# Optimization experiments

Hardware: AMD Instinct MI355X
Metric: run time of the kernel (lower is better)

Reference implementation:

```python
import jax, jax.numpy as jnp
import numpy as np
from jax import lax

NL, HID, DIN, DST, DCONV, DTR = 4, 256, 512, 16, 4, 16  # layers, d_model, expand*d_model, d_state, d_conv, dt_rank
B, H, W = 4, 256, 256


def setup_inputs() -> dict:
    key = jax.random.key(0)
    ks = jax.random.split(key, 8)
    def n(k, s, sc=0.02):
        return jax.random.normal(k, s, dtype=jnp.float32) * sc
    return {
        "x": jax.random.normal(ks[0], (B, 3, H, W), dtype=jnp.float32),
        "conv1_w": n(ks[1], (HID // 2, 3, 3, 3), 0.1), "conv1_b": jnp.zeros((HID // 2,), jnp.float32),
        "gn1_w": jnp.ones((HID // 2,), jnp.float32), "gn1_b": jnp.zeros((HID // 2,), jnp.float32),
        "conv2_w": n(ks[2], (HID, HID // 2, 3, 3), 0.05), "conv2_b": jnp.zeros((HID,), jnp.float32),
        "gn2_w": jnp.ones((HID,), jnp.float32), "gn2_b": jnp.zeros((HID,), jnp.float32),
        "ln_w": jnp.ones((NL, HID), jnp.float32), "ln_b": jnp.zeros((NL, HID), jnp.float32),
        "in_proj_w": n(ks[3], (NL, 2 * DIN, HID)),
        "conv1d_w": n(ks[4], (NL, DIN, 1, DCONV), 0.1), "conv1d_b": jnp.zeros((NL, DIN), jnp.float32),
        "x_proj_w": n(ks[5], (NL, DTR + 2 * DST, DIN)),
        "dt_proj_w": n(ks[6], (NL, DIN, DTR), 0.1),
        "dt_proj_b": jnp.full((NL, DIN), -4.6, dtype=jnp.float32),  # softplus(-4.6) ~ 0.01
        "A_log": jnp.broadcast_to(jnp.log(jnp.arange(1, DST + 1, dtype=jnp.float32)), (NL, DIN, DST)) + jnp.zeros((NL, DIN, DST), jnp.float32),
        "D": jnp.ones((NL, DIN), jnp.float32),
        "out_proj_w": n(ks[7], (NL, HID, DIN)),
    }


def conv2d_s2(x, w, b):
    y = lax.conv_general_dilated(x, w, (2, 2), [(1, 1), (1, 1)],
                                 dimension_numbers=('NCHW', 'OIHW', 'NCHW'))
    return y + b[None, :, None, None]


def group_norm(x, w, b, groups=8, eps=1e-5):
    Bb, C, Hh, Ww = x.shape
    xg = x.reshape(Bb, groups, C // groups, Hh, Ww)
    m = xg.mean((2, 3, 4), keepdims=True)
    v = xg.var((2, 3, 4), keepdims=True)
    xg = (xg - m) * lax.rsqrt(v + eps)
    return xg.reshape(Bb, C, Hh, Ww) * w[None, :, None, None] + b[None, :, None, None]


def layer_norm(x, w, b, eps=1e-5):
    m = x.mean(-1, keepdims=True)
    v = x.var(-1, keepdims=True)
    return (x - m) * lax.rsqrt(v + eps) * w + b


def mamba(x, ipw, cw, cb, xpw, dpw, dpb, A_log, Dp, opw):
    # x: [B, L, HID]
    Bb, L, _ = x.shape
    xz = jnp.einsum('bld,ed->ble', x, ipw)           # [B, L, 2*DIN]
    xc, z = jnp.split(xz, 2, axis=-1)
    # depthwise causal conv1d over L
    u = xc.transpose(0, 2, 1)                        # [B, DIN, L]
    u = lax.conv_general_dilated(u, cw, (1,), [(DCONV - 1, 0)],
                                 dimension_numbers=('NCH', 'OIH', 'NCH'),
                                 feature_group_count=DIN)
    xc = jax.nn.silu(u + cb[None, :, None]).transpose(0, 2, 1)  # [B, L, DIN]
    x_dbl = jnp.einsum('bld,ed->ble', xc, xpw)       # [B, L, DTR+2*DST]
    dt, Bm, Cm = jnp.split(x_dbl, [DTR, DTR + DST], axis=-1)
    delta = jax.nn.softplus(jnp.einsum('blr,dr->bld', dt, dpw) + dpb)  # [B, L, DIN]
    A = -jnp.exp(A_log)                              # [DIN, DST]
    dA = jnp.exp(jnp.einsum('bld,dn->bldn', delta, A))
    dBu = jnp.einsum('bld,bln,bld->bldn', delta, Bm, xc)

    def step(h, inp):
        dA_t, dBu_t, C_t = inp
        h = dA_t * h + dBu_t                         # [B, DIN, DST]
        return h, jnp.einsum('bdn,bn->bd', h, C_t)

    h0 = jnp.zeros((Bb, DIN, DST), x.dtype)
    _, ys = lax.scan(step, h0, (dA.transpose(1, 0, 2, 3), dBu.transpose(1, 0, 2, 3), Cm.transpose(1, 0, 2)))
    y = ys.transpose(1, 0, 2) + xc * Dp              # [B, L, DIN]
    y = y * jax.nn.silu(z)
    return jnp.einsum('bld,ed->ble', y, opw)         # [B, L, HID]


def reference(x, conv1_w, conv1_b, gn1_w, gn1_b, conv2_w, conv2_b, gn2_w, gn2_b,
              ln_w, ln_b, in_proj_w, conv1d_w, conv1d_b, x_proj_w, dt_proj_w,
              dt_proj_b, A_log, D, out_proj_w):
    y = jax.nn.silu(group_norm(conv2d_s2(x, conv1_w, conv1_b), gn1_w, gn1_b))
    y = jax.nn.silu(group_norm(conv2d_s2(y, conv2_w, conv2_b), gn2_w, gn2_b))
    Bb, C, h, w = y.shape
    s = y.reshape(Bb, C, h * w).transpose(0, 2, 1)   # b (h w) c
    for i in range(NL):
        s = s + mamba(layer_norm(s, ln_w[i], ln_b[i]), in_proj_w[i], conv1d_w[i],
                      conv1d_b[i], x_proj_w[i], dt_proj_w[i], dt_proj_b[i],
                      A_log[i], D[i], out_proj_w[i])
    return (s, h, w)
```

## Files before the change

### kernel.cpp

```cpp
#include <hip/hip_runtime.h>
#include <math.h>

#define BB 4
#define C1 128
#define H1 128
#define W1 128
#define C2 256
#define H2 64
#define W2 64
#define LSEQ 4096
#define HID 256
#define DIN 512
#define DST 16
#define DTR 16
#define NL 4
#define NCHUNK 128
#define LCH 32

typedef unsigned short u16;
using short8 = __attribute__((ext_vector_type(8))) short;
using f32x4  = __attribute__((ext_vector_type(4))) float;
using f32x2  = __attribute__((ext_vector_type(2))) float;

static __device__ __forceinline__ float dsilu(float x){
    return x / (1.0f + __expf(-x));
}
static __device__ __forceinline__ u16 f2bf(float f){
    unsigned u = __float_as_uint(f);
    u += 0x7FFF + ((u >> 16) & 1);
    return (u16)(u >> 16);
}
static __device__ __forceinline__ float bf2f(u16 v){
    return __uint_as_float(((unsigned)v) << 16);
}

#define GLL16(g, l) __builtin_amdgcn_global_load_lds( \
    (const __attribute__((address_space(1))) void*)(g), \
    (__attribute__((address_space(3))) void*)(l), 16, 0, 0)

#define VMW4 asm volatile("s_waitcnt vmcnt(4)" ::: "memory")
#define VMW5 asm volatile("s_waitcnt vmcnt(5)" ::: "memory")
#define VMW0 asm volatile("s_waitcnt vmcnt(0)" ::: "memory")

static __device__ __forceinline__ void blockbar(){
    asm volatile("" ::: "memory");
    __builtin_amdgcn_s_barrier();
    asm volatile("" ::: "memory");
}

__global__ void f2bf_kernel(const float* __restrict__ src, u16* __restrict__ dst){
    int idx = blockIdx.x * 256 + threadIdx.x;
    dst[idx] = f2bf(src[idx]);
}
__global__ void wdt_prep_kernel(const float* __restrict__ xpw, const float* __restrict__ dpw,
                                u16* __restrict__ wcomb){
    int idx = blockIdx.x * 256 + threadIdx.x;
    int k = idx & 511;
    int n = (idx >> 9) % 640;
    int layer = idx / (640*512);
    u16 val = 0;
    if(n < 512){
        const float* dp = dpw + ((long)layer*512 + n)*16;
        const float* xp = xpw + (long)layer*48*512 + k;
        float acc = 0.f;
        #pragma unroll
        for(int r = 0; r < 16; ++r) acc = fmaf(dp[r], xp[(long)r*512], acc);
        val = f2bf(acc);
    } else if(n < 544){
        int row = n - 512 + 16;
        val = f2bf(xpw[((long)layer*48 + row)*512 + k]);
    }
    wcomb[((long)layer*640 + n)*512 + k] = val;
}
__global__ void c2w_prep_kernel(const float* __restrict__ src, u16* __restrict__ dst){
    int idx = blockIdx.x * 256 + threadIdx.x;
    int ci = idx & 127, p = (idx >> 7) % 9, co = idx / (9*128);
    int kh = p / 3, kw = p - 3*kh;
    dst[idx] = f2bf(src[((co*128 + ci)*3 + kh)*3 + kw]);
}
__global__ void xt_zero_kernel(unsigned* __restrict__ xt){
    xt[blockIdx.x * 256 + threadIdx.x] = 0;
}

__global__ __launch_bounds__(256) void conv1_kernel(
        const float* __restrict__ x, const float* __restrict__ w,
        const float* __restrict__ bias, float* __restrict__ y){
    __shared__ float xs[9][260];
    int oh = blockIdx.x, b = blockIdx.y;
    int tid = threadIdx.x;
    #pragma unroll
    for(int r = 0; r < 9; ++r){
        int ci = r / 3, kh = r - 3*ci;
        int ih = 2*oh - 1 + kh;
        float v = 0.f;
        if(ih >= 0) v = x[((b*3 + ci)*256 + ih)*256 + tid];
        xs[r][tid + 1] = v;
        if(tid == 0) xs[r][0] = 0.f;
    }
    __syncthreads();
    int co = tid >> 1, h = tid & 1;
    float wr[27];
    #pragma unroll
    for(int j = 0; j < 27; ++j) wr[j] = w[co*27 + j];
    float bz = bias[co];
    long obase = ((long)((b*128 + co)*128 + oh))*128 + h*64;
    #pragma unroll 4
    for(int i = 0; i < 64; ++i){
        int iw0 = 2*(h*64 + i);
        float acc = bz;
        #pragma unroll
        for(int r = 0; r < 9; ++r){
            acc = fmaf(xs[r][iw0+0], wr[r*3+0], acc);
            acc = fmaf(xs[r][iw0+1], wr[r*3+1], acc);
            acc = fmaf(xs[r][iw0+2], wr[r*3+2], acc);
        }
        y[obase + i] = acc;
    }
}

__global__ void zero_stats_kernel(float* __restrict__ stats){
    stats[threadIdx.x] = 0.0f;
}

__global__ void gn_stats_kernel(const float* __restrict__ x, float* __restrict__ stats,
                                int elems_per_group){
    const int EPB = 16384;
    long base = (long)blockIdx.x * EPB;
    int g = (int)(base / elems_per_group);
    float s = 0.f, ss = 0.f;
    for(int j = threadIdx.x; j < EPB; j += 256){
        float v = x[base + j];
        s += v; ss += v*v;
    }
    #pragma unroll
    for(int off = 32; off; off >>= 1){
        s  += __shfl_down(s,  off);
        ss += __shfl_down(ss, off);
    }
    __shared__ float ls[4], lss[4];
    int wid = threadIdx.x >> 6, lane = threadIdx.x & 63;
    if(lane == 0){ ls[wid] = s; lss[wid] = ss; }
    __syncthreads();
    if(threadIdx.x == 0){
        atomicAdd(&stats[g],      ls[0]+ls[1]+ls[2]+ls[3]);
        atomicAdd(&stats[32+g], lss[0]+lss[1]+lss[2]+lss[3]);
    }
}

__global__ void gn1_transform_kernel(const float* __restrict__ y1, const float* __restrict__ stats,
                                     const float* __restrict__ w, const float* __restrict__ bias,
                                     u16* __restrict__ xt){
    __shared__ float tile[32][33];
    int b = blockIdx.z >> 7, ih = blockIdx.z & 127;
    int c0 = blockIdx.y * 32, w0 = blockIdx.x * 32;
    int tx = threadIdx.x, ty = threadIdx.y;
    const float cnt = 16.f * 128.f * 128.f;
    #pragma unroll
    for(int i = 0; i < 4; ++i){
        int ci = c0 + ty + i*8;
        int g = b*8 + (ci >> 4);
        float mean = stats[g] / cnt;
        float var  = stats[32+g] / cnt - mean*mean;
        float rstd = rsqrtf(var + 1e-5f);
        float v = y1[(((long)(b*C1 + ci))*H1 + ih)*W1 + w0 + tx];
        tile[ty + i*8][tx] = dsilu((v - mean) * rstd * w[ci] + bias[ci]);
    }
    __syncthreads();
    #pragma unroll
    for(int i = 0; i < 4; ++i){
        int iwl = ty + i*8;
        xt[((long)(b*130 + ih + 1)*130 + (w0 + iwl + 1))*128 + c0 + tx] = f2bf(tile[tx][iwl]);
    }
}

__global__ __launch_bounds__(256) void conv2gemm_bf16_kernel(
        const u16* __restrict__ xt, const u16* __restrict__ w2,
        const float* __restrict__ bias, float* __restrict__ y2t){
    __shared__ u16 Asm[2][128*32];
    __shared__ u16 Bsm[2][128*32];
    int m0 = blockIdx.x * 128, n0 = blockIdx.y * 128;
    int tid = threadIdx.x;
    long abase[2]; const u16* bbase[2]; int ldst[2];
    #pragma unroll
    for(int it = 0; it < 2; ++it){
        int c = it*256 + tid;
        int r = c >> 2;
        int kq = ((c & 3) ^ ((r >> 1) & 3)) * 8;
        int m = m0 + r;
        int b = m >> 12, oh = (m >> 6) & 63, ow = m & 63;
        abase[it] = ((long)(b*130 + 2*oh)*130 + 2*ow)*128 + kq;
        bbase[it] = w2 + (long)(n0 + r)*1152 + kq;
        ldst[it] = c*8;
    }
    int wave = tid >> 6, lane = tid & 63;
    int wr = wave >> 1, wc = wave & 1;
    int lm = lane & 15, lq = lane >> 4;
    int swq = (lq ^ ((lm >> 1) & 3)) * 8;
    f32x4 acc[4][4] = {};
    #pragma unroll
    for(int it = 0; it < 2; ++it){
        GLL16(xt + abase[it], &Asm[0][ldst[it]]);
        GLL16(bbase[it], &Bsm[0][ldst[it]]);
    }
    for(int kk = 0; kk < 36; ++kk){
        int cur = kk & 1;
        if(kk + 1 < 36){
            int k2 = kk + 1;
            int p = k2 >> 2, cs = k2 & 3;
            int kh = p / 3, kw = p - 3*kh;
            int ao = (kh*130 + kw)*128 + cs*32;
            int bo = k2*32;
            #pragma unroll
            for(int it = 0; it < 2; ++it){
                GLL16(xt + abase[it] + ao, &Asm[cur^1][ldst[it]]);
                GLL16(bbase[it] + bo, &Bsm[cur^1][ldst[it]]);
            }
            VMW4;
        } else {
            VMW0;
        }
        blockbar();
        short8 af[4], bf[4];
        #pragma unroll
        for(int i = 0; i < 4; ++i){
            af[i] = *(const short8*)&Asm[cur][(wr*64 + i*16 + lm)*32 + swq];
            bf[i] = *(const short8*)&Bsm[cur][(wc*64 + i*16 + lm)*32 + swq];
        }
        #pragma unroll
        for(int i = 0; i < 4; ++i)
            #pragma unroll
            for(int j = 0; j < 4; ++j)
                acc[i][j] = __builtin_amdgcn_mfma_f32_16x16x32_bf16(af[i], bf[j], acc[i][j], 0, 0, 0);
        __builtin_amdgcn_sched_barrier(0);
        blockbar();
    }
    #pragma unroll
    for(int i = 0; i < 4; ++i){
        long row = m0 + wr*64 + i*16 + lq*4;
        #pragma unroll
        for(int j = 0; j < 4; ++j){
            int col = n0 + wc*64 + j*16 + lm;
            float bz = bias[col];
            #pragma unroll
            for(int r = 0; r < 4; ++r)
                y2t[(row + r)*256L + col] = acc[i][j][r] + bz;
        }
    }
}

__global__ void gn2t_stats_kernel(const float* __restrict__ y2t, float* __restrict__ stats){
    int b = blockIdx.y;
    long row0 = (long)b*LSEQ + blockIdx.x*64;
    int c = threadIdx.x;
    float s = 0.f, ss = 0.f;
    for(int r = 0; r < 64; ++r){
        float v = y2t[(row0 + r)*C2 + c];
        s += v; ss += v*v;
    }
    #pragma unroll
    for(int off = 16; off; off >>= 1){
        s  += __shfl_down(s,  off);
        ss += __shfl_down(ss, off);
    }
    if((c & 31) == 0){
        int g = b*8 + (c >> 5);
        atomicAdd(&stats[g], s);
        atomicAdd(&stats[32+g], ss);
    }
}

__global__ void gn2t_apply_ln_kernel(const float* __restrict__ y2t, const float* __restrict__ stats,
                                     const float* __restrict__ gw, const float* __restrict__ gb,
                                     const float* __restrict__ lw, const float* __restrict__ lb,
                                     float* __restrict__ s, u16* __restrict__ xln){
    long row = blockIdx.x;
    int c = threadIdx.x;
    int b = (int)(row >> 12);
    int g = b*8 + (c >> 5);
    const float cnt = 32.f * (float)LSEQ;
    float mean = stats[g] / cnt;
    float var  = stats[32+g] / cnt - mean*mean;
    float rstd = rsqrtf(var + 1e-5f);
    float v = dsilu((y2t[row*HID + c] - mean) * rstd * gw[c] + gb[c]);
    s[row*HID + c] = v;
    float sm = v, sq = v*v;
    #pragma unroll
    for(int off = 32; off; off >>= 1){
        sm += __shfl_down(sm, off);
        sq += __shfl_down(sq, off);
    }
    __shared__ float pa[4], pb[4], res[2];
    int wid = c >> 6, lane = c & 63;
    if(lane == 0){ pa[wid] = sm; pb[wid] = sq; }
    __syncthreads();
    if(c == 0){
        float t  = pa[0]+pa[1]+pa[2]+pa[3];
        float tt = pb[0]+pb[1]+pb[2]+pb[3];
        float m2 = t / 256.f;
        float v2 = tt / 256.f - m2*m2;
        res[0] = m2; res[1] = rsqrtf(v2 + 1e-5f);
    }
    __syncthreads();
    xln[row*HID + c] = f2bf((v - res[0]) * res[1] * lw[c] + lb[c]);
}

__global__ __launch_bounds__(256) void gemm_bf16_kernel(
        const u16* __restrict__ A, const u16* __restrict__ B, void* __restrict__ Cv,
        int K, int Nact, int ldc, int mode){
    __shared__ u16 Asm[2][128*32];
    __shared__ u16 Bsm[2][128*32];
    int m0 = blockIdx.x * 128, n0 = blockIdx.y * 128;
    int tid = threadIdx.x;
    int wave = tid >> 6, lane = tid & 63;
    int wr = wave >> 1, wc = wave & 1;
    int lm = lane & 15, lq = lane >> 4;
    int swq = (lq ^ ((lm >> 1) & 3)) * 8;
    const u16* ag[2]; const u16* bg[2]; int ldst[2];
    #pragma unroll
    for(int it = 0; it < 2; ++it){
        int c = it*256 + tid;
        int r = c >> 2;
        int kq = ((c & 3) ^ ((r >> 1) & 3)) * 8;
        ag[it] = A + (long)(m0 + r)*K + kq;
        bg[it] = B + (long)(n0 + r)*K + kq;
        ldst[it] = c*8;
    }
    f32x4 acc[4][4] = {};
    int nk = K >> 5;
    #pragma unroll
    for(int it = 0; it < 2; ++it){
        GLL16(ag[it], &Asm[0][ldst[it]]);
        GLL16(bg[it], &Bsm[0][ldst[it]]);
    }
    for(int kt = 0; kt < nk; ++kt){
        int cur = kt & 1;
        if(kt + 1 < nk){
            int ko = (kt + 1) << 5;
            #pragma unroll
            for(int it = 0; it < 2; ++it){
                GLL16(ag[it] + ko, &Asm[cur^1][ldst[it]]);
                GLL16(bg[it] + ko, &Bsm[cur^1][ldst[it]]);
            }
            VMW4;
        } else {
            VMW0;
        }
        blockbar();
        short8 af[4], bf[4];
        #pragma unroll
        for(int i = 0; i < 4; ++i){
            af[i] = *(const short8*)&Asm[cur][(wr*64 + i*16 + lm)*32 + swq];
            bf[i] = *(const short8*)&Bsm[cur][(wc*64 + i*16 + lm)*32 + swq];
        }
        #pragma unroll
        for(int i = 0; i < 4; ++i)
            #pragma unroll
            for(int j = 0; j < 4; ++j)
                acc[i][j] = __builtin_amdgcn_mfma_f32_16x16x32_bf16(af[i], bf[j], acc[i][j], 0, 0, 0);
        __builtin_amdgcn_sched_barrier(0);
        blockbar();
    }
    #pragma unroll
    for(int i = 0; i < 4; ++i){
        long row = m0 + wr*64 + i*16 + lq*4;
        #pragma unroll
        for(int j = 0; j < 4; ++j){
            int col = n0 + wc*64 + j*16 + lm;
            if(col < Nact){
                #pragma unroll
                for(int r = 0; r < 4; ++r){
                    long idx = (row + r)*(long)ldc + col;
                    if(mode == 2) ((u16*)Cv)[idx] = f2bf(acc[i][j][r]);
                    else          ((float*)Cv)[idx] = acc[i][j][r];
                }
            }
        }
    }
}

__global__ __launch_bounds__(256) void gemm_dtbc_kernel(
        const u16* __restrict__ A, const u16* __restrict__ B,
        const float* __restrict__ dpb, u16* __restrict__ dv,
        float* __restrict__ xdbl32){
    __shared__ u16 Asm[2][128*32];
    __shared__ u16 Bsm[2][128*32];
    int m0 = blockIdx.x * 128, n0 = blockIdx.y * 128;
    int tid = threadIdx.x;
    int wave = tid >> 6, lane = tid & 63;
    int wr = wave >> 1, wc = wave & 1;
    int lm = lane & 15, lq = lane >> 4;
    int swq = (lq ^ ((lm >> 1) & 3)) * 8;
    const u16* ag[2]; const u16* bg[2]; int ldst[2];
    #pragma unroll
    for(int it = 0; it < 2; ++it){
        int c = it*256 + tid;
        int r = c >> 2;
        int kq = ((c & 3) ^ ((r >> 1) & 3)) * 8;
        ag[it] = A + (long)(m0 + r)*512 + kq;
        bg[it] = B + (long)(n0 + r)*512 + kq;
        ldst[it] = c*8;
    }
    f32x4 acc[4][4] = {};
    #pragma unroll
    for(int it = 0; it < 2; ++it){
        GLL16(ag[it], &Asm[0][ldst[it]]);
        GLL16(bg[it], &Bsm[0][ldst[it]]);
    }
    for(int kt = 0; kt < 16; ++kt){
        int cur = kt & 1;
        if(kt + 1 < 16){
            int ko = (kt + 1) << 5;
            #pragma unroll
            for(int it = 0; it < 2; ++it){
                GLL16(ag[it] + ko, &Asm[cur^1][ldst[it]]);
                GLL16(bg[it] + ko, &Bsm[cur^1][ldst[it]]);
            }
            VMW4;
        } else {
            VMW0;
        }
        blockbar();
        short8 af[4], bf[4];
        #pragma unroll
        for(int i = 0; i < 4; ++i){
            af[i] = *(const short8*)&Asm[cur][(wr*64 + i*16 + lm)*32 + swq];
            bf[i] = *(const short8*)&Bsm[cur][(wc*64 + i*16 + lm)*32 + swq];
        }
        #pragma unroll
        for(int i = 0; i < 4; ++i)
            #pragma unroll
            for(int j = 0; j < 4; ++j)
                acc[i][j] = __builtin_amdgcn_mfma_f32_16x16x32_bf16(af[i], bf[j], acc[i][j], 0, 0, 0);
        __builtin_amdgcn_sched_barrier(0);
        blockbar();
    }
    if(n0 < 512){
        #pragma unroll
        for(int i = 0; i < 4; ++i){
            long row = m0 + wr*64 + i*16 + lq*4;
            #pragma unroll
            for(int j = 0; j < 4; ++j){
                int col = n0 + wc*64 + j*16 + lm;
                float bz = dpb[col];
                #pragma unroll
                for(int r = 0; r < 4; ++r){
                    float v = acc[i][j][r] + bz;
                    v = (v > 20.f) ? v : __logf(1.f + __expf(v));
                    dv[(row + r)*512L + col] = f2bf(v);
                }
            }
        }
    } else {
        #pragma unroll
        for(int i = 0; i < 4; ++i){
            long row = m0 + wr*64 + i*16 + lq*4;
            #pragma unroll
            for(int j = 0; j < 4; ++j){
                int lcol = wc*64 + j*16 + lm;
                if(lcol < 32){
                    #pragma unroll
                    for(int r = 0; r < 4; ++r)
                        xdbl32[(row + r)*32L + lcol] = acc[i][j][r];
                }
            }
        }
    }
}

__global__ __launch_bounds__(256) void gemm_out_ln_kernel(
        const u16* __restrict__ A, const u16* __restrict__ B,
        float* __restrict__ s, u16* __restrict__ xln,
        const float* __restrict__ lw, const float* __restrict__ lb){
    __shared__ u16 Asm[2][64*32];
    __shared__ u16 Bsm[2][256*32];
    int m0 = blockIdx.x * 64;
    int tid = threadIdx.x;
    int w = tid >> 6, lane = tid & 63;
    int lm = lane & 15, lq = lane >> 4;
    int swq = (lq ^ ((lm >> 1) & 3)) * 8;
    int ra = tid >> 2;
    int kqa = ((tid & 3) ^ ((ra >> 1) & 3)) * 8;
    const u16* agA = A + (long)(m0 + ra)*512 + kqa;
    int lda = tid*8;
    const u16* bg[4]; int ldb[4];
    #pragma unroll
    for(int it = 0; it < 4; ++it){
        int c = it*256 + tid;
        int r = c >> 2;
        int kq = ((c & 3) ^ ((r >> 1) & 3)) * 8;
        bg[it] = B + (long)r*512 + kq;
        ldb[it] = c*8;
    }
    f32x4 acc[16] = {};
    GLL16(agA, &Asm[0][lda]);
    #pragma unroll
    for(int it = 0; it < 4; ++it)
        GLL16(bg[it], &Bsm[0][ldb[it]]);
    for(int kt = 0; kt < 16; ++kt){
        int cur = kt & 1;
        if(kt + 1 < 16){
            int ko = (kt + 1) << 5;
            GLL16(agA + ko, &Asm[cur^1][lda]);
            #pragma unroll
            for(int it = 0; it < 4; ++it)
                GLL16(bg[it] + ko, &Bsm[cur^1][ldb[it]]);
            VMW5;
        } else {
            VMW0;
        }
        blockbar();
        short8 af = *(const short8*)&Asm[cur][(w*16 + lm)*32 + swq];
        #pragma unroll
        for(int j = 0; j < 16; ++j){
            short8 bf = *(const short8*)&Bsm[cur][(j*16 + lm)*32 + swq];
            acc[j] = __builtin_amdgcn_mfma_f32_16x16x32_bf16(af, bf, acc[j], 0, 0, 0);
        }
        __builtin_amdgcn_sched_barrier(0);
        blockbar();
    }
    int row0 = m0 + w*16 + lq*4;
    float psum[4] = {0.f,0.f,0.f,0.f}, psq[4] = {0.f,0.f,0.f,0.f};
    #pragma unroll
    for(int j = 0; j < 16; ++j){
        int col = j*16 + lm;
        #pragma unroll
        for(int r = 0; r < 4; ++r){
            long idx = (long)(row0 + r)*HID + col;
            float v = s[idx] + acc[j][r];
            acc[j][r] = v;
            s[idx] = v;
            psum[r] += v; psq[r] += v*v;
        }
    }
    #pragma unroll
    for(int mask = 1; mask <= 8; mask <<= 1){
        #pragma unroll
        for(int r = 0; r < 4; ++r){
            psum[r] += __shfl_xor(psum[r], mask);
            psq[r]  += __shfl_xor(psq[r],  mask);
        }
    }
    float mean[4], rstd[4];
    #pragma unroll
    for(int r = 0; r < 4; ++r){
        mean[r] = psum[r] * (1.f/256.f);
        float var = psq[r] * (1.f/256.f) - mean[r]*mean[r];
        rstd[r] = rsqrtf(var + 1e-5f);
    }
    #pragma unroll
    for(int j = 0; j < 16; ++j){
        int col = j*16 + lm;
        float wv = lw[col], bv = lb[col];
        #pragma unroll
        for(int r = 0; r < 4; ++r){
            long idx = (long)(row0 + r)*HID + col;
            xln[idx] = f2bf((acc[j][r] - mean[r]) * rstd[r] * wv + bv);
        }
    }
}

__global__ void conv1d_silu_kernel(const u16* __restrict__ xz, const float* __restrict__ w,
                                   const float* __restrict__ bias, u16* __restrict__ xcv){
    int idx = blockIdx.x * 256 + threadIdx.x;
    int e = idx * 8;
    int d0 = e & 511;
    long m = e >> 9;
    int l = (int)(m & 4095);
    short8 xrow[4];
    const u16* xp = xz + m*(2*DIN) + d0;
    #pragma unroll
    for(int j = 0; j < 4; ++j){
        int t = l - 3 + j;
        if(t >= 0) xrow[j] = *(const short8*)(xp + (long)(j-3)*(2*DIN));
        else       xrow[j] = (short8){0,0,0,0,0,0,0,0};
    }
    float wv[8][4];
    #pragma unroll
    for(int k = 0; k < 8; k += 2){
        float4 a = *(const float4*)(w + (d0+k)*4);
        float4 b = *(const float4*)(w + (d0+k+1)*4);
        wv[k][0]=a.x; wv[k][1]=a.y; wv[k][2]=a.z; wv[k][3]=a.w;
        wv[k+1][0]=b.x; wv[k+1][1]=b.y; wv[k+1][2]=b.z; wv[k+1][3]=b.w;
    }
    float bz[8];
    {
        float4 a = *(const float4*)(bias + d0);
        float4 b = *(const float4*)(bias + d0 + 4);
        bz[0]=a.x; bz[1]=a.y; bz[2]=a.z; bz[3]=a.w;
        bz[4]=b.x; bz[5]=b.y; bz[6]=b.z; bz[7]=b.w;
    }
    short8 out;
    #pragma unroll
    for(int k = 0; k < 8; ++k){
        float acc = bz[k];
        #pragma unroll
        for(int j = 0; j < 4; ++j)
            acc = fmaf(bf2f((u16)xrow[j][k]), wv[k][j], acc);
        out[k] = (short)f2bf(dsilu(acc));
    }
    *(short8*)(xcv + m*DIN + d0) = out;
}

__global__ __launch_bounds__(256) void scan1_kernel(
        const u16* __restrict__ xcvb, const u16* __restrict__ dvin,
        const float* __restrict__ xdbl32, const float* __restrict__ Alog,
        float* __restrict__ aprod, float* __restrict__ hend){
    int d = blockIdx.y * 256 + threadIdx.x;
    int c = blockIdx.x;
    int b = blockIdx.z;
    __shared__ float bm[LCH][16];
    {
        int t = threadIdx.x >> 4, n = threadIdx.x & 15;
        #pragma unroll
        for(int it = 0; it < 2; ++it){
            long p = ((long)(b*LSEQ + c*LCH + t + it*16))*32;
            bm[t + it*16][n] = xdbl32[p + n];
        }
    }
    __syncthreads();
    float An[16];
    #pragma unroll
    for(int n = 0; n < 16; ++n)
        An[n] = -__expf(Alog[d*16 + n]);
    float An0 = An[0];
    bool structural = true;
    #pragma unroll
    for(int n = 0; n < 16; ++n)
        structural = structural && (fabsf(An[n] - (float)(n+1)*An0) <= 1e-3f*(float)(n+1));
    long base = ((long)(b*LSEQ + c*LCH))*DIN + d;
    long ob = (((long)(b*NCHUNK + c))*DIN + d)*16;
    if(structural){
        f32x2 h2[8];
        #pragma unroll
        for(int i = 0; i < 8; ++i) h2[i] = (f32x2){0.f, 0.f};
        float sumdv = 0.f;
        float xv_n = bf2f(xcvb[base]);
        float dv_n = bf2f(dvin[base]);
        for(int t = 0; t < LCH; ++t){
            float xv = xv_n, dv = dv_n;
            if(t + 1 < LCH){
                xv_n = bf2f(xcvb[base + (long)(t+1)*DIN]);
                dv_n = bf2f(dvin[base + (long)(t+1)*DIN]);
            }
            sumdv += dv;
            float db = dv * xv;
            float r1 = __expf(dv * An0);
            float r2 = r1 * r1;
            f32x2 rr = {r2, r2};
            f32x2 e2[8];
            e2[0] = (f32x2){r1, r2};
            #pragma unroll
            for(int i = 1; i < 8; ++i) e2[i] = e2[i-1] * rr;
            f32x2 db2 = {db, db};
            const f32x2* b2 = (const f32x2*)&bm[t][0];
            #pragma unroll
            for(int i = 0; i < 8; ++i) h2[i] = e2[i]*h2[i] + db2*b2[i];
        }
        float R = __expf(An0 * sumdv);
        float Rp = R;
        const float* hp = (const float*)h2;
        #pragma unroll
        for(int n = 0; n < 16; ++n){
            aprod[ob+n] = Rp; Rp *= R;
            hend[ob+n] = hp[n];
        }
    } else {
        float h[16], ap[16];
        #pragma unroll
        for(int n = 0; n < 16; ++n){ h[n] = 0.f; ap[n] = 1.f; }
        for(int t = 0; t < LCH; ++t){
            float dv = bf2f(dvin[base + (long)t*DIN]);
            float db = dv * bf2f(xcvb[base + (long)t*DIN]);
            #pragma unroll
            for(int n = 0; n < 16; ++n){
                float e = __expf(dv * An[n]);
                ap[n] *= e;
                h[n] = fmaf(e, h[n], db * bm[t][n]);
            }
        }
        #pragma unroll
        for(int n = 0; n < 16; ++n){ aprod[ob+n] = ap[n]; hend[ob+n] = h[n]; }
    }
}

__global__ void scan2_kernel(const float* __restrict__ aprod, const float* __restrict__ hend,
                             float* __restrict__ hinit){
    int idx = blockIdx.x * 256 + threadIdx.x;
    int n = idx & 15, d = (idx >> 4) & 511, b = idx >> 13;
    const long stride = (long)DIN * 16;
    long p0 = (((long)(b*NCHUNK))*DIN + d)*16 + n;
    float h = 0.f;
    for(int c = 0; c < NCHUNK; c += 8){
        float a[8], e[8];
        #pragma unroll
        for(int j = 0; j < 8; ++j){
            long p = p0 + (long)(c + j)*stride;
            a[j] = aprod[p]; e[j] = hend[p];
        }
        #pragma unroll
        for(int j = 0; j < 8; ++j){
            hinit[p0 + (long)(c + j)*stride] = h;
            h = fmaf(a[j], h, e[j]);
        }
    }
}

__global__ __launch_bounds__(256) void scan3_kernel(
        const u16* __restrict__ xcvb, const u16* __restrict__ dvin,
        const float* __restrict__ xdbl32, const float* __restrict__ Alog,
        const float* __restrict__ hinit, const float* __restrict__ Dp,
        const u16* __restrict__ xz, u16* __restrict__ yout){
    int d = blockIdx.y * 256 + threadIdx.x;
    int c = blockIdx.x;
    int b = blockIdx.z;
    __shared__ float bm[LCH][16], cm[LCH][16];
    {
        int t = threadIdx.x >> 4, n = threadIdx.x & 15;
        #pragma unroll
        for(int it = 0; it < 2; ++it){
            long p = ((long)(b*LSEQ + c*LCH + t + it*16))*32;
            bm[t + it*16][n] = xdbl32[p + n];
            cm[t + it*16][n] = xdbl32[p + 16 + n];
        }
    }
    __syncthreads();
    float An[16];
    long hb = (((long)(b*NCHUNK + c))*DIN + d)*16;
    #pragma unroll
    for(int n = 0; n < 16; ++n)
        An[n] = -__expf(Alog[d*16 + n]);
    float An0 = An[0];
    bool structural = true;
    #pragma unroll
    for(int n = 0; n < 16; ++n)
        structural = structural && (fabsf(An[n] - (float)(n+1)*An0) <= 1e-3f*(float)(n+1));
    float Dv = Dp[d];
    long base  = ((long)(b*LSEQ + c*LCH))*DIN + d;
    long zbase = ((long)(b*LSEQ + c*LCH))*(2*DIN) + DIN + d;
    if(structural){
        f32x2 h2[8];
        {
            const f32x2* hi = (const f32x2*)&hinit[hb];
            #pragma unroll
            for(int i = 0; i < 8; ++i) h2[i] = hi[i];
        }
        float xv_n = bf2f(xcvb[base]);
        float z_n  = bf2f(xz[zbase]);
        float dv_n = bf2f(dvin[base]);
        for(int t = 0; t < LCH; ++t){
            float xv = xv_n, z = z_n, dv = dv_n;
            if(t + 1 < LCH){
                xv_n = bf2f(xcvb[base + (long)(t+1)*DIN]);
                z_n  = bf2f(xz[zbase + (long)(t+1)*(2*DIN)]);
                dv_n = bf2f(dvin[base + (long)(t+1)*DIN]);
            }
            float db = dv * xv;
            float r1 = __expf(dv * An0);
            float r2 = r1 * r1;
            f32x2 rr = {r2, r2};
            f32x2 e2[8];
            e2[0] = (f32x2){r1, r2};
            #pragma unroll
            for(int i = 1; i < 8; ++i) e2[i] = e2[i-1] * rr;
            f32x2 db2 = {db, db};
            const f32x2* b2 = (const f32x2*)&bm[t][0];
            const f32x2* c2 = (const f32x2*)&cm[t][0];
            f32x2 y2 = {0.f, 0.f};
            #pragma unroll
            for(int i = 0; i < 8; ++i){
                h2[i] = e2[i]*h2[i] + db2*b2[i];
                y2 = y2 + h2[i]*c2[i];
            }
            float y = y2[0] + y2[1];
            y = fmaf(xv, Dv, y);
            yout[base + (long)t*DIN] = f2bf(y * dsilu(z));
        }
    } else {
        float h[16];
        #pragma unroll
        for(int n = 0; n < 16; ++n) h[n] = hinit[hb + n];
        for(int t = 0; t < LCH; ++t){
            float dv = bf2f(dvin[base + (long)t*DIN]);
            float xv = bf2f(xcvb[base + (long)t*DIN]);
            float db = dv * xv;
            float y = 0.f;
            #pragma unroll
            for(int n = 0; n < 16; ++n){
                float e = __expf(dv * An[n]);
                h[n] = fmaf(e, h[n], db * bm[t][n]);
                y = fmaf(h[n], cm[t][n], y);
            }
            y = fmaf(xv, Dv, y);
            float z = bf2f(xz[zbase + (long)t*(2*DIN)]);
            yout[base + (long)t*DIN] = f2bf(y * dsilu(z));
        }
    }
}

__global__ void copyout_kernel(const float* __restrict__ s, float* __restrict__ out, int out_size){
    int idx = blockIdx.x * 256 + threadIdx.x;
    if(idx >= out_size) return;
    out[idx] = (idx < BB*LSEQ*HID) ? s[idx] : 64.0f;
}

extern "C" void kernel_launch(void* const* d_in, const int* in_sizes, int n_in,
                              void* d_out, int out_size, void* d_ws, size_t ws_size,
                              hipStream_t stream){
    const float* x        = (const float*)d_in[0];
    const float* conv1_w  = (const float*)d_in[1];
    const float* conv1_b  = (const float*)d_in[2];
    const float* gn1_w    = (const float*)d_in[3];
    const float* gn1_b    = (const float*)d_in[4];
    const float* conv2_w  = (const float*)d_in[5];
    const float* conv2_b  = (const float*)d_in[6];
    const float* gn2_w    = (const float*)d_in[7];
    const float* gn2_b    = (const float*)d_in[8];
    const float* ln_w     = (const float*)d_in[9];
    const float* ln_b     = (const float*)d_in[10];
    const float* in_proj  = (const float*)d_in[11];
    const float* c1d_w    = (const float*)d_in[12];
    const float* c1d_b    = (const float*)d_in[13];
    const float* x_proj   = (const float*)d_in[14];
    const float* dt_w     = (const float*)d_in[15];
    const float* dt_b     = (const float*)d_in[16];
    const float* A_log    = (const float*)d_in[17];
    const float* Dvec     = (const float*)d_in[18];
    const float* out_proj = (const float*)d_in[19];

    float* ws = (float*)d_ws;
    float* s      = ws;
    u16*   xz_bf  = (u16*)(ws + 4194304);
    float* y1     = ws + 4194304;
    u16*   xt     = (u16*)(ws + 12582912);
    u16*   xcv_bf = (u16*)(ws + 16909312);
    float* y2t    = ws + 16909312;
    u16*   xln_bf = (u16*)(ws + 21103616);
    float* xdbl   = ws + 23200768;
    float* aprod  = ws + 23987200;
    float* hendb  = ws + 28181504;
    u16*   y_bf   = (u16*)aprod;
    float* hinit  = ws + 32375808;
    float* stats  = ws + 36570112;
    u16*   ipw_bf = (u16*)(ws + 36570176);
    u16*   opw_bf = ipw_bf + 1048576;
    u16*   c2w_bf = opw_bf + 524288;
    u16*   dv_bf  = (u16*)(ws + 37635200);
    u16*   wcomb  = (u16*)(ws + 41829504);

    f2bf_kernel<<<4096, 256, 0, stream>>>(in_proj, ipw_bf);
    f2bf_kernel<<<2048, 256, 0, stream>>>(out_proj, opw_bf);
    c2w_prep_kernel<<<1152, 256, 0, stream>>>(conv2_w, c2w_bf);
    wdt_prep_kernel<<<5120, 256, 0, stream>>>(x_proj, dt_w, wcomb);

    conv1_kernel<<<dim3(128,4), 256, 0, stream>>>(x, conv1_w, conv1_b, y1);
    zero_stats_kernel<<<1, 64, 0, stream>>>(stats);
    gn_stats_kernel<<<512, 256, 0, stream>>>(y1, stats, 16*H1*W1);
    xt_zero_kernel<<<16900, 256, 0, stream>>>((unsigned*)xt);
    gn1_transform_kernel<<<dim3(4,4,512), dim3(32,8), 0, stream>>>(y1, stats, gn1_w, gn1_b, xt);
    conv2gemm_bf16_kernel<<<dim3(128,2), 256, 0, stream>>>(xt, c2w_bf, conv2_b, y2t);
    zero_stats_kernel<<<1, 64, 0, stream>>>(stats);
    gn2t_stats_kernel<<<dim3(64,4), 256, 0, stream>>>(y2t, stats);
    gn2t_apply_ln_kernel<<<16384, 256, 0, stream>>>(y2t, stats, gn2_w, gn2_b,
                                                    ln_w, ln_b, s, xln_bf);

    for(int layer = 0; layer < NL; ++layer){
        const float* cw  = c1d_w + (long)layer*DIN*4;
        const float* cb  = c1d_b + (long)layer*DIN;
        const float* dpb = dt_b  + (long)layer*DIN;
        const float* Al  = A_log + (long)layer*DIN*DST;
        const float* Dl  = Dvec  + (long)layer*DIN;
        int lnext = (layer + 1) & 3;

        gemm_bf16_kernel<<<dim3(128,8), 256, 0, stream>>>(
            xln_bf, ipw_bf + (long)layer*1024*256, xz_bf, HID, 2*DIN, 2*DIN, 2);
        conv1d_silu_kernel<<<4096, 256, 0, stream>>>(xz_bf, cw, cb, xcv_bf);
        gemm_dtbc_kernel<<<dim3(128,5), 256, 0, stream>>>(
            xcv_bf, wcomb + (long)layer*640*512, dpb, dv_bf, xdbl);
        scan1_kernel<<<dim3(NCHUNK,2,BB), 256, 0, stream>>>(
            xcv_bf, dv_bf, xdbl, Al, aprod, hendb);
        scan2_kernel<<<128, 256, 0, stream>>>(aprod, hendb, hinit);
        scan3_kernel<<<dim3(NCHUNK,2,BB), 256, 0, stream>>>(
            xcv_bf, dv_bf, xdbl, Al, hinit, Dl, xz_bf, y_bf);
        gemm_out_ln_kernel<<<256, 256, 0, stream>>>(
            y_bf, opw_bf + (long)layer*256*512, s, xln_bf,
            ln_w + lnext*HID, ln_b + lnext*HID);
    }

    copyout_kernel<<<(out_size + 255)/256, 256, 0, stream>>>(s, (float*)d_out, out_size);
}
```

Baseline: 845.2 us.

## Triple-buffer GEMM pipelines, shrink tiles, enlarge scan chunks, zero only padding border

All bf16 GEMM kernels move from double to triple LDS buffering, issuing loads two k-steps ahead with matching vmcnt waits. The conv2 GEMM and the out-projection+LayerNorm GEMM use smaller M tiles so more blocks launch; the latter now reduces LN statistics across waves through shared memory. The selective-scan chunk length doubles (64 chunks of 64), which halves the chunk count for the inter-chunk pass. The full zero fill of the padded conv2 input is replaced by zeroing only the border cells. Together these aim to hide memory latency, raise occupancy and cut redundant writes, at the cost of more LDS per block and more per-chunk serial scan work.

Result: faster. 783.7 us (-7.3%).

```diff
diff --git a/kernel.cpp b/kernel.cpp
--- a/kernel.cpp
+++ b/kernel.cpp
@@ -14,8 +14,8 @@
 #define DST 16
 #define DTR 16
 #define NL 4
-#define NCHUNK 128
-#define LCH 32
+#define NCHUNK 64
+#define LCH 64
 
 typedef unsigned short u16;
 using short8 = __attribute__((ext_vector_type(8))) short;
@@ -37,10 +37,11 @@
 #define GLL16(g, l) __builtin_amdgcn_global_load_lds( \
     (const __attribute__((address_space(1))) void*)(g), \
     (__attribute__((address_space(3))) void*)(l), 16, 0, 0)
-
-#define VMW4 asm volatile("s_waitcnt vmcnt(4)" ::: "memory")
-#define VMW5 asm volatile("s_waitcnt vmcnt(5)" ::: "memory")
-#define VMW0 asm volatile("s_waitcnt vmcnt(0)" ::: "memory")
+#define GLL4(g, l) __builtin_amdgcn_global_load_lds( \
+    (const __attribute__((address_space(1))) void*)(g), \
+    (__attribute__((address_space(3))) void*)(l), 4, 0, 0)
+
+#define VMW(n) asm volatile("s_waitcnt vmcnt(" #n ")" ::: "memory")
 
 static __device__ __forceinline__ void blockbar(){
     asm volatile("" ::: "memory");
@@ -78,8 +79,17 @@
     int kh = p / 3, kw = p - 3*kh;
     dst[idx] = f2bf(src[((co*128 + ci)*3 + kh)*3 + kw]);
 }
-__global__ void xt_zero_kernel(unsigned* __restrict__ xt){
-    xt[blockIdx.x * 256 + threadIdx.x] = 0;
+__global__ void xt_border_kernel(unsigned* __restrict__ xt){
+    int idx = blockIdx.x * 256 + threadIdx.x;
+    int c2 = idx & 63;
+    int cell = (idx >> 6) % 516;
+    int b = idx / (516*64);
+    int ih, iw;
+    if(cell < 130){ ih = 0; iw = cell; }
+    else if(cell < 260){ ih = 129; iw = cell - 130; }
+    else if(cell < 388){ iw = 0; ih = cell - 259; }
+    else { iw = 129; ih = cell - 387; }
+    xt[((long)(b*130 + ih)*130 + iw)*64 + c2] = 0;
 }
 
 __global__ __launch_bounds__(256) void conv1_kernel(
@@ -176,58 +186,71 @@
 __global__ __launch_bounds__(256) void conv2gemm_bf16_kernel(
         const u16* __restrict__ xt, const u16* __restrict__ w2,
         const float* __restrict__ bias, float* __restrict__ y2t){
-    __shared__ u16 Asm[2][128*32];
-    __shared__ u16 Bsm[2][128*32];
-    int m0 = blockIdx.x * 128, n0 = blockIdx.y * 128;
+    __shared__ u16 Asm[3][64*32];
+    __shared__ u16 Bsm[3][128*32];
+    int m0 = blockIdx.x * 64, n0 = blockIdx.y * 128;
     int tid = threadIdx.x;
-    long abase[2]; const u16* bbase[2]; int ldst[2];
+    long abase;
+    {
+        int r = tid >> 2;
+        int kq = ((tid & 3) ^ ((r >> 1) & 3)) * 8;
+        int m = m0 + r;
+        int b = m >> 12, oh = (m >> 6) & 63, ow = m & 63;
+        abase = ((long)(b*130 + 2*oh)*130 + 2*ow)*128 + kq;
+    }
+    int lda = tid*8;
+    const u16* bbase[2]; int ldb[2];
     #pragma unroll
     for(int it = 0; it < 2; ++it){
         int c = it*256 + tid;
         int r = c >> 2;
         int kq = ((c & 3) ^ ((r >> 1) & 3)) * 8;
-        int m = m0 + r;
-        int b = m >> 12, oh = (m >> 6) & 63, ow = m & 63;
-        abase[it] = ((long)(b*130 + 2*oh)*130 + 2*ow)*128 + kq;
         bbase[it] = w2 + (long)(n0 + r)*1152 + kq;
-        ldst[it] = c*8;
+        ldb[it] = c*8;
     }
     int wave = tid >> 6, lane = tid & 63;
     int wr = wave >> 1, wc = wave & 1;
     int lm = lane & 15, lq = lane >> 4;
     int swq = (lq ^ ((lm >> 1) & 3)) * 8;
-    f32x4 acc[4][4] = {};
-    #pragma unroll
-    for(int it = 0; it < 2; ++it){
-        GLL16(xt + abase[it], &Asm[0][ldst[it]]);
-        GLL16(bbase[it], &Bsm[0][ldst[it]]);
+    f32x4 acc[2][4] = {};
+    #pragma unroll
+    for(int pt = 0; pt < 2; ++pt){
+        int p = pt >> 2, cs = pt & 3;
+        int kh = p / 3, kw = p - 3*kh;
+        int ao = (kh*130 + kw)*128 + cs*32;
+        GLL16(xt + abase + ao, &Asm[pt][lda]);
+        #pragma unroll
+        for(int it = 0; it < 2; ++it)
+            GLL16(bbase[it] + pt*32, &Bsm[pt][ldb[it]]);
     }
     for(int kk = 0; kk < 36; ++kk){
-        int cur = kk & 1;
-        if(kk + 1 < 36){
-            int k2 = kk + 1;
+        int cur = kk % 3;
+        if(kk + 2 < 36){
+            int k2 = kk + 2;
+            int nxt = (kk + 2) % 3;
             int p = k2 >> 2, cs = k2 & 3;
             int kh = p / 3, kw = p - 3*kh;
             int ao = (kh*130 + kw)*128 + cs*32;
-            int bo = k2*32;
-            #pragma unroll
-            for(int it = 0; it < 2; ++it){
-                GLL16(xt + abase[it] + ao, &Asm[cur^1][ldst[it]]);
-                GLL16(bbase[it] + bo, &Bsm[cur^1][ldst[it]]);
-            }
-            VMW4;
+            GLL16(xt + abase + ao, &Asm[nxt][lda]);
+            #pragma unroll
+            for(int it = 0; it < 2; ++it)
+                GLL16(bbase[it] + k2*32, &Bsm[nxt][ldb[it]]);
+            VMW(6);
+        } else if(kk + 1 < 36){
+            VMW(3);
         } else {
-            VMW0;
+            VMW(0);
         }
         blockbar();
-        short8 af[4], bf[4];
-        #pragma unroll
-        for(int i = 0; i < 4; ++i){
-            af[i] = *(const short8*)&Asm[cur][(wr*64 + i*16 + lm)*32 + swq];
-            bf[i] = *(const short8*)&Bsm[cur][(wc*64 + i*16 + lm)*32 + swq];
-        }
-        #pragma unroll
-        for(int i = 0; i < 4; ++i)
+        short8 af[2], bf[4];
+        #pragma unroll
+        for(int i = 0; i < 2; ++i)
+            af[i] = *(const short8*)&Asm[cur][(wr*32 + i*16 + lm)*32 + swq];
+        #pragma unroll
+        for(int j = 0; j < 4; ++j)
+            bf[j] = *(const short8*)&Bsm[cur][(wc*64 + j*16 + lm)*32 + swq];
+        #pragma unroll
+        for(int i = 0; i < 2; ++i)
             #pragma unroll
             for(int j = 0; j < 4; ++j)
                 acc[i][j] = __builtin_amdgcn_mfma_f32_16x16x32_bf16(af[i], bf[j], acc[i][j], 0, 0, 0);
@@ -235,8 +258,8 @@
         blockbar();
     }
     #pragma unroll
-    for(int i = 0; i < 4; ++i){
-        long row = m0 + wr*64 + i*16 + lq*4;
+    for(int i = 0; i < 2; ++i){
+        long row = m0 + wr*32 + i*16 + lq*4;
         #pragma unroll
         for(int j = 0; j < 4; ++j){
             int col = n0 + wc*64 + j*16 + lm;
@@ -307,8 +330,8 @@
 __global__ __launch_bounds__(256) void gemm_bf16_kernel(
         const u16* __restrict__ A, const u16* __restrict__ B, void* __restrict__ Cv,
         int K, int Nact, int ldc, int mode){
-    __shared__ u16 Asm[2][128*32];
-    __shared__ u16 Bsm[2][128*32];
+    __shared__ u16 Asm[3][128*32];
+    __shared__ u16 Bsm[3][128*32];
     int m0 = blockIdx.x * 128, n0 = blockIdx.y * 128;
     int tid = threadIdx.x;
     int wave = tid >> 6, lane = tid & 63;
@@ -328,22 +351,29 @@
     f32x4 acc[4][4] = {};
     int nk = K >> 5;
     #pragma unroll
-    for(int it = 0; it < 2; ++it){
-        GLL16(ag[it], &Asm[0][ldst[it]]);
-        GLL16(bg[it], &Bsm[0][ldst[it]]);
+    for(int pt = 0; pt < 2; ++pt){
+        int ko = pt << 5;
+        #pragma unroll
+        for(int it = 0; it < 2; ++it){
+            GLL16(ag[it] + ko, &Asm[pt][ldst[it]]);
+            GLL16(bg[it] + ko, &Bsm[pt][ldst[it]]);
+        }
     }
     for(int kt = 0; kt < nk; ++kt){
-        int cur = kt & 1;
-        if(kt + 1 < nk){
-            int ko = (kt + 1) << 5;
+        int cur = kt % 3;
+        if(kt + 2 < nk){
+            int nxt = (kt + 2) % 3;
+            int ko = (kt + 2) << 5;
             #pragma unroll
             for(int it = 0; it < 2; ++it){
-                GLL16(ag[it] + ko, &Asm[cur^1][ldst[it]]);
-                GLL16(bg[it] + ko, &Bsm[cur^1][ldst[it]]);
+                GLL16(ag[it] + ko, &Asm[nxt][ldst[it]]);
+                GLL16(bg[it] + ko, &Bsm[nxt][ldst[it]]);
             }
-            VMW4;
+            VMW(8);
+        } else if(kt + 1 < nk){
+            VMW(4);
         } else {
-            VMW0;
+            VMW(0);
         }
         blockbar();
         short8 af[4], bf[4];
@@ -382,8 +412,8 @@
         const u16* __restrict__ A, const u16* __restrict__ B,
         const float* __restrict__ dpb, u16* __restrict__ dv,
         float* __restrict__ xdbl32){
-    __shared__ u16 Asm[2][128*32];
-    __shared__ u16 Bsm[2][128*32];
+    __shared__ u16 Asm[3][128*32];
+    __shared__ u16 Bsm[3][128*32];
     int m0 = blockIdx.x * 128, n0 = blockIdx.y * 128;
     int tid = threadIdx.x;
     int wave = tid >> 6, lane = tid & 63;
@@ -402,22 +432,29 @@
     }
     f32x4 acc[4][4] = {};
     #pragma unroll
-    for(int it = 0; it < 2; ++it){
-        GLL16(ag[it], &Asm[0][ldst[it]]);
-        GLL16(bg[it], &Bsm[0][ldst[it]]);
+    for(int pt = 0; pt < 2; ++pt){
+        int ko = pt << 5;
+        #pragma unroll
+        for(int it = 0; it < 2; ++it){
+            GLL16(ag[it] + ko, &Asm[pt][ldst[it]]);
+            GLL16(bg[it] + ko, &Bsm[pt][ldst[it]]);
+        }
     }
     for(int kt = 0; kt < 16; ++kt){
-        int cur = kt & 1;
-        if(kt + 1 < 16){
-            int ko = (kt + 1) << 5;
+        int cur = kt % 3;
+        if(kt + 2 < 16){
+            int nxt = (kt + 2) % 3;
+            int ko = (kt + 2) << 5;
             #pragma unroll
             for(int it = 0; it < 2; ++it){
-                GLL16(ag[it] + ko, &Asm[cur^1][ldst[it]]);
-                GLL16(bg[it] + ko, &Bsm[cur^1][ldst[it]]);
+                GLL16(ag[it] + ko, &Asm[nxt][ldst[it]]);
+                GLL16(bg[it] + ko, &Bsm[nxt][ldst[it]]);
             }
-            VMW4;
+            VMW(8);
+        } else if(kt + 1 < 16){
+            VMW(4);
         } else {
-            VMW0;
+            VMW(0);
         }
         blockbar();
         short8 af[4], bf[4];
@@ -471,17 +508,25 @@
         const u16* __restrict__ A, const u16* __restrict__ B,
         float* __restrict__ s, u16* __restrict__ xln,
         const float* __restrict__ lw, const float* __restrict__ lb){
-    __shared__ u16 Asm[2][64*32];
-    __shared__ u16 Bsm[2][256*32];
-    int m0 = blockIdx.x * 64;
+    __shared__ u16 Asm[3][32*32];
+    __shared__ u16 Bsm[3][256*32];
+    __shared__ float lnred[2][2][16][2];
+    int m0 = blockIdx.x * 32;
     int tid = threadIdx.x;
-    int w = tid >> 6, lane = tid & 63;
+    int wave = tid >> 6, lane = tid & 63;
+    int wr = wave >> 1, wc = wave & 1;
     int lm = lane & 15, lq = lane >> 4;
     int swq = (lq ^ ((lm >> 1) & 3)) * 8;
-    int ra = tid >> 2;
-    int kqa = ((tid & 3) ^ ((ra >> 1) & 3)) * 8;
-    const u16* agA = A + (long)(m0 + ra)*512 + kqa;
-    int lda = tid*8;
+    const u16* agA[2]; int lda[2];
+    #pragma unroll
+    for(int it = 0; it < 2; ++it){
+        int c = it*256 + tid;
+        int r = c >> 4;
+        int kp = (c & 15) * 2;
+        int kel = ((((c & 15) >> 2) ^ ((r >> 1) & 3)) << 3) + (kp & 7);
+        agA[it] = A + (long)(m0 + r)*512 + kel;
+        lda[it] = c*2;
+    }
     const u16* bg[4]; int ldb[4];
     #pragma unroll
     for(int it = 0; it < 4; ++it){
@@ -491,38 +536,45 @@
         bg[it] = B + (long)r*512 + kq;
         ldb[it] = c*8;
     }
-    f32x4 acc[16] = {};
-    GLL16(agA, &Asm[0][lda]);
-    #pragma unroll
-    for(int it = 0; it < 4; ++it)
-        GLL16(bg[it], &Bsm[0][ldb[it]]);
+    f32x4 acc[8] = {};
+    #pragma unroll
+    for(int pt = 0; pt < 2; ++pt){
+        int ko = pt << 5;
+        #pragma unroll
+        for(int it = 0; it < 2; ++it) GLL4(agA[it] + ko, &Asm[pt][lda[it]]);
+        #pragma unroll
+        for(int it = 0; it < 4; ++it) GLL16(bg[it] + ko, &Bsm[pt][ldb[it]]);
+    }
     for(int kt = 0; kt < 16; ++kt){
-        int cur = kt & 1;
-        if(kt + 1 < 16){
-            int ko = (kt + 1) << 5;
-            GLL16(agA + ko, &Asm[cur^1][lda]);
-            #pragma unroll
-            for(int it = 0; it < 4; ++it)
-                GLL16(bg[it] + ko, &Bsm[cur^1][ldb[it]]);
-            VMW5;
+        int cur = kt % 3;
+        if(kt + 2 < 16){
+            int nxt = (kt + 2) % 3;
+            int ko = (kt + 2) << 5;
+            #pragma unroll
+            for(int it = 0; it < 2; ++it) GLL4(agA[it] + ko, &Asm[nxt][lda[it]]);
+            #pragma unroll
+            for(int it = 0; it < 4; ++it) GLL16(bg[it] + ko, &Bsm[nxt][ldb[it]]);
+            VMW(12);
+        } else if(kt + 1 < 16){
+            VMW(6);
         } else {
-            VMW0;
+            VMW(0);
         }
         blockbar();
-        short8 af = *(const short8*)&Asm[cur][(w*16 + lm)*32 + swq];
-        #pragma unroll
-        for(int j = 0; j < 16; ++j){
-            short8 bf = *(const short8*)&Bsm[cur][(j*16 + lm)*32 + swq];
+        short8 af = *(const short8*)&Asm[cur][(wr*16 + lm)*32 + swq];
+        #pragma unroll
+        for(int j = 0; j < 8; ++j){
+            short8 bf = *(const short8*)&Bsm[cur][(wc*128 + j*16 + lm)*32 + swq];
             acc[j] = __builtin_amdgcn_mfma_f32_16x16x32_bf16(af, bf, acc[j], 0, 0, 0);
         }
         __builtin_amdgcn_sched_barrier(0);
         blockbar();
     }
-    int row0 = m0 + w*16 + lq*4;
+    int row0 = m0 + wr*16 + lq*4;
     float psum[4] = {0.f,0.f,0.f,0.f}, psq[4] = {0.f,0.f,0.f,0.f};
     #pragma unroll
-    for(int j = 0; j < 16; ++j){
-        int col = j*16 + lm;
+    for(int j = 0; j < 8; ++j){
+        int col = wc*128 + j*16 + lm;
         #pragma unroll
         for(int r = 0; r < 4; ++r){
             long idx = (long)(row0 + r)*HID + col;
@@ -540,16 +592,26 @@
             psq[r]  += __shfl_xor(psq[r],  mask);
         }
     }
+    if(lm == 0){
+        #pragma unroll
+        for(int r = 0; r < 4; ++r){
+            lnred[wr][wc][lq*4 + r][0] = psum[r];
+            lnred[wr][wc][lq*4 + r][1] = psq[r];
+        }
+    }
+    __syncthreads();
     float mean[4], rstd[4];
     #pragma unroll
     for(int r = 0; r < 4; ++r){
-        mean[r] = psum[r] * (1.f/256.f);
-        float var = psq[r] * (1.f/256.f) - mean[r]*mean[r];
+        float t  = lnred[wr][0][lq*4 + r][0] + lnred[wr][1][lq*4 + r][0];
+        float tt = lnred[wr][0][lq*4 + r][1] + lnred[wr][1][lq*4 + r][1];
+        mean[r] = t * (1.f/256.f);
+        float var = tt * (1.f/256.f) - mean[r]*mean[r];
         rstd[r] = rsqrtf(var + 1e-5f);
     }
     #pragma unroll
-    for(int j = 0; j < 16; ++j){
-        int col = j*16 + lm;
+    for(int j = 0; j < 8; ++j){
+        int col = wc*128 + j*16 + lm;
         float wv = lw[col], bv = lb[col];
         #pragma unroll
         for(int r = 0; r < 4; ++r){
@@ -612,7 +674,7 @@
     {
         int t = threadIdx.x >> 4, n = threadIdx.x & 15;
         #pragma unroll
-        for(int it = 0; it < 2; ++it){
+        for(int it = 0; it < 4; ++it){
             long p = ((long)(b*LSEQ + c*LCH + t + it*16))*32;
             bm[t + it*16][n] = xdbl32[p + n];
         }
@@ -717,7 +779,7 @@
     {
         int t = threadIdx.x >> 4, n = threadIdx.x & 15;
         #pragma unroll
-        for(int it = 0; it < 2; ++it){
+        for(int it = 0; it < 4; ++it){
             long p = ((long)(b*LSEQ + c*LCH + t + it*16))*32;
             bm[t + it*16][n] = xdbl32[p + n];
             cm[t + it*16][n] = xdbl32[p + 16 + n];
@@ -855,9 +917,9 @@
     conv1_kernel<<<dim3(128,4), 256, 0, stream>>>(x, conv1_w, conv1_b, y1);
     zero_stats_kernel<<<1, 64, 0, stream>>>(stats);
     gn_stats_kernel<<<512, 256, 0, stream>>>(y1, stats, 16*H1*W1);
-    xt_zero_kernel<<<16900, 256, 0, stream>>>((unsigned*)xt);
+    xt_border_kernel<<<516, 256, 0, stream>>>((unsigned*)xt);
     gn1_transform_kernel<<<dim3(4,4,512), dim3(32,8), 0, stream>>>(y1, stats, gn1_w, gn1_b, xt);
-    conv2gemm_bf16_kernel<<<dim3(128,2), 256, 0, stream>>>(xt, c2w_bf, conv2_b, y2t);
+    conv2gemm_bf16_kernel<<<dim3(256,2), 256, 0, stream>>>(xt, c2w_bf, conv2_b, y2t);
     zero_stats_kernel<<<1, 64, 0, stream>>>(stats);
     gn2t_stats_kernel<<<dim3(64,4), 256, 0, stream>>>(y2t, stats);
     gn2t_apply_ln_kernel<<<16384, 256, 0, stream>>>(y2t, stats, gn2_w, gn2_b,
@@ -881,7 +943,7 @@
         scan2_kernel<<<128, 256, 0, stream>>>(aprod, hendb, hinit);
         scan3_kernel<<<dim3(NCHUNK,2,BB), 256, 0, stream>>>(
             xcv_bf, dv_bf, xdbl, Al, hinit, Dl, xz_bf, y_bf);
-        gemm_out_ln_kernel<<<256, 256, 0, stream>>>(
+        gemm_out_ln_kernel<<<512, 256, 0, stream>>>(
             y_bf, opw_bf + (long)layer*256*512, s, xln_bf,
             ln_w + lnext*HID, ln_b + lnext*HID);
     }
```
